# Kernel tuning notes

Measured on AMD Instinct MI355X. Metric: run time of the kernel, lower is better.

Reference implementation:

```python
import jax, jax.numpy as jnp
import numpy as np

B, S, T = 128, 512, 128
E, He, Ed, H = 512, 512, 512, 512


def setup_inputs() -> dict:
    key = jax.random.key(0)
    ks = jax.random.split(key, 13)
    w = lambda k, shape: jax.random.normal(k, shape, jnp.float32) * 0.02
    return {
        "trg_embed": jax.random.normal(ks[0], (B, T, E), jnp.float32),
        "edit_representation_final": jax.random.normal(ks[1], (1, B, 2 * Ed), jnp.float32),
        "edit_representation_cell_state": jax.random.normal(ks[2], (1, B, 2 * Ed), jnp.float32),
        "encoder_hidden": jax.random.normal(ks[3], (B, S, 2 * He), jnp.float32),
        "encoder_final": jax.random.normal(ks[4], (1, B, 2 * He), jnp.float32),
        "encoder_cell_state": jax.random.normal(ks[5], (1, B, 2 * He), jnp.float32),
        "src_mask": jnp.ones((B, 1, S), dtype=bool),
        "W_key": w(ks[6], (2 * He, H)),
        "W_query": w(ks[7], (H, H)),
        "w_energy": w(ks[8], (H,)),
        "W_bridge": w(ks[9], (2 * He + 2 * Ed, H)),
        "b_bridge": jnp.zeros((H,), jnp.float32),
        "W_ih": w(ks[10], (4 * H, E + 2 * He + 2 * Ed)),
        "W_hh": w(ks[11], (4 * H, H)),
        "b_ih": jnp.zeros((4 * H,), jnp.float32),
        "b_hh": jnp.zeros((4 * H,), jnp.float32),
        "W_pre": w(ks[12], (H, H + 2 * He + E)),
    }


def reference(trg_embed, edit_representation_final, edit_representation_cell_state,
              encoder_hidden, encoder_final, encoder_cell_state, src_mask,
              W_key, W_query, w_energy, W_bridge, b_bridge,
              W_ih, W_hh, b_ih, b_hh, W_pre):
    # bridge: init hidden / cell from final encoder + edit states  [1,B,H]
    h0 = jnp.tanh(jnp.concatenate([encoder_final, edit_representation_final], -1) @ W_bridge + b_bridge)
    c0 = jnp.tanh(jnp.concatenate([encoder_cell_state, edit_representation_cell_state], -1) @ W_bridge + b_bridge)
    proj_key = encoder_hidden @ W_key              # [B,S,H] (computed once)
    edit_flat = edit_representation_final[0]       # [B,2*Ed]
    mask = src_mask[:, 0, :]                       # [B,S]
    bias = b_ih + b_hh

    def step(carry, x_t):
        h, c = carry                               # [B,H] each
        # Bahdanau attention
        q = h @ W_query                            # [B,H]
        scores = jnp.tanh(q[:, None, :] + proj_key) @ w_energy   # [B,S]
        scores = jnp.where(mask, scores, -jnp.inf)
        alphas = jax.nn.softmax(scores, axis=-1)
        context = jnp.einsum('bs,bsd->bd', alphas, encoder_hidden)  # [B,2*He]
        # LSTM cell (torch gate order: i, f, g, o)
        rnn_in = jnp.concatenate([x_t, context, edit_flat], -1)
        gates = rnn_in @ W_ih.T + h @ W_hh.T + bias
        i_g, f_g, g_g, o_g = jnp.split(gates, 4, axis=-1)
        c_new = jax.nn.sigmoid(f_g) * c + jax.nn.sigmoid(i_g) * jnp.tanh(g_g)
        h_new = jax.nn.sigmoid(o_g) * jnp.tanh(c_new)
        # pre-output projection (dropout in eval mode = identity)
        pre = jnp.concatenate([x_t, h_new, context], -1) @ W_pre.T
        return (h_new, c_new), (h_new, pre)

    (h_last, c_last), (states, pre_outs) = jax.lax.scan(
        step, (h0[0], c0[0]), jnp.swapaxes(trg_embed, 0, 1))
    decoder_states = jnp.swapaxes(states, 0, 1)       # [B,T,H]
    pre_output_vectors = jnp.swapaxes(pre_outs, 0, 1) # [B,T,H]
    return decoder_states, h_last[None], pre_output_vectors
```

## Files before the change

kernel.cpp:

```cpp
#include <hip/hip_runtime.h>
#include <hip/hip_bf16.h>

typedef unsigned short u16;
typedef unsigned int u32;
typedef unsigned char u8;

typedef __attribute__((ext_vector_type(8))) __bf16 bf16x8;
typedef __attribute__((ext_vector_type(4))) float f32x4;
typedef __attribute__((ext_vector_type(2))) float f32x2;

__device__ __forceinline__ float fast_tanh(float x){
    float e = __expf(2.0f*x);
    return 1.0f - 2.0f/(e+1.0f);
}
__device__ __forceinline__ float fast_sigmoid(float x){
    return 1.0f/(1.0f+__expf(-x));
}
__device__ __forceinline__ float bflo(u32 u){ return __uint_as_float(u<<16); }
__device__ __forceinline__ float bfhi(u32 u){ return __uint_as_float(u & 0xffff0000u); }
__device__ __forceinline__ float bf2f(u16 u){ return __uint_as_float(((u32)u)<<16); }
__device__ __forceinline__ u16 f2bf(float v){
    __hip_bfloat16 h = __float2bfloat16(v);
    return *reinterpret_cast<u16*>(&h);
}
__device__ __forceinline__ f32x2 fp8lo(u32 u){ return __builtin_amdgcn_cvt_pk_f32_fp8(u, false); }
__device__ __forceinline__ f32x2 fp8hi(u32 u){ return __builtin_amdgcn_cvt_pk_f32_fp8(u, true); }

__device__ __forceinline__ void gridbar(int* cnt, int* gate, int e){
    __syncthreads();
    if (threadIdx.x == 0){
        int prev = __hip_atomic_fetch_add(cnt, 1, __ATOMIC_ACQ_REL, __HIP_MEMORY_SCOPE_AGENT);
        if (prev == e*256 - 1)
            __hip_atomic_store(gate, e, __ATOMIC_RELEASE, __HIP_MEMORY_SCOPE_AGENT);
        while (__hip_atomic_load(gate, __ATOMIC_RELAXED, __HIP_MEMORY_SCOPE_AGENT) < e)
            __builtin_amdgcn_s_sleep(8);
        (void)__hip_atomic_load(gate, __ATOMIC_ACQUIRE, __HIP_MEMORY_SCOPE_AGENT);
    }
    __syncthreads();
}

__device__ __forceinline__ void pairbar(int* pflags, int e){
    __syncthreads();
    if (threadIdx.x == 0){
        __hip_atomic_store(&pflags[blockIdx.x*32], e, __ATOMIC_RELEASE, __HIP_MEMORY_SCOPE_AGENT);
        int partner = (blockIdx.x ^ 1)*32;
        while (__hip_atomic_load(&pflags[partner], __ATOMIC_RELAXED, __HIP_MEMORY_SCOPE_AGENT) < e)
            __builtin_amdgcn_s_sleep(2);
        (void)__hip_atomic_load(&pflags[partner], __ATOMIC_ACQUIRE, __HIP_MEMORY_SCOPE_AGENT);
    }
    __syncthreads();
}

template<int C_MODE, int HAS_BIAS>
__global__ __launch_bounds__(256) void mfma_gemm(
    const u16* __restrict__ A, int lda,
    const u16* __restrict__ Bw, int ldb,
    const float* __restrict__ bias,
    void* __restrict__ Cp, long ldc, int K)
{
    __shared__ u16 Ash[128*64];
    __shared__ u16 Bsh[128*64];
    const int tid  = threadIdx.x;
    const int w    = tid >> 6;
    const int lane = tid & 63;
    const int wr   = w >> 1, wc = w & 1;
    const int row0 = blockIdx.y * 128, col0 = blockIdx.x * 128;

    f32x4 acc[4][4];
    #pragma unroll
    for (int i = 0; i < 4; i++)
        #pragma unroll
        for (int j = 0; j < 4; j++)
            acc[i][j] = f32x4{0.f,0.f,0.f,0.f};

    for (int k0 = 0; k0 < K; k0 += 64) {
        #pragma unroll
        for (int it = 0; it < 4; it++) {
            int j = it*256 + tid;
            int row = j >> 3, s = j & 7;
            const u16* src = A + (size_t)(row0 + row) * lda + k0 + ((s ^ (row & 7)) << 3);
            __builtin_amdgcn_global_load_lds(
                (const __attribute__((address_space(1))) unsigned int*)src,
                (__attribute__((address_space(3))) unsigned int*)(Ash + (size_t)(it*256 + w*64)*8),
                16, 0, 0);
        }
        #pragma unroll
        for (int it = 0; it < 4; it++) {
            int j = it*256 + tid;
            int row = j >> 3, s = j & 7;
            const u16* src = Bw + (size_t)(col0 + row) * ldb + k0 + ((s ^ (row & 7)) << 3);
            __builtin_amdgcn_global_load_lds(
                (const __attribute__((address_space(1))) unsigned int*)src,
                (__attribute__((address_space(3))) unsigned int*)(Bsh + (size_t)(it*256 + w*64)*8),
                16, 0, 0);
        }
        __syncthreads();
        #pragma unroll
        for (int kh = 0; kh < 2; kh++) {
            bf16x8 af[4], bg[4];
            #pragma unroll
            for (int f = 0; f < 4; f++) {
                int row = wr*64 + f*16 + (lane & 15);
                int slot = (kh*4 + (lane >> 4)) ^ (row & 7);
                af[f] = *(const bf16x8*)(Ash + row*64 + slot*8);
                int nn = wc*64 + f*16 + (lane & 15);
                int slot2 = (kh*4 + (lane >> 4)) ^ (nn & 7);
                bg[f] = *(const bf16x8*)(Bsh + nn*64 + slot2*8);
            }
            #pragma unroll
            for (int fm = 0; fm < 4; fm++)
                #pragma unroll
                for (int fn = 0; fn < 4; fn++)
                    acc[fm][fn] = __builtin_amdgcn_mfma_f32_16x16x32_bf16(af[fm], bg[fn], acc[fm][fn], 0, 0, 0);
        }
        __syncthreads();
    }

    #pragma unroll
    for (int fm = 0; fm < 4; fm++) {
        #pragma unroll
        for (int fn = 0; fn < 4; fn++) {
            int col = col0 + wc*64 + fn*16 + (lane & 15);
            #pragma unroll
            for (int r = 0; r < 4; r++) {
                int row = row0 + wr*64 + fm*16 + ((lane >> 4)<<2) + r;
                float v = acc[fm][fn][r];
                if (HAS_BIAS) v += bias[col];
                if (C_MODE == 1)
                    ((u16*)Cp)[(size_t)row * ldc + col] = f2bf(v);
                else
                    ((float*)Cp)[(((size_t)(row & 127)) << 16) + ((size_t)(row >> 7) << 9) + col] = v;
            }
        }
    }
}

__global__ __launch_bounds__(512, 1) void k_mega(
    u16* __restrict__ pre_in,
    const u16* __restrict__ Wq_t,
    const u8*  __restrict__ pk8,
    const float* __restrict__ we_g,
    const u8*  __restrict__ enc8,
    const u16* __restrict__ Wg,
    const u16* __restrict__ edit_part,
    u16* __restrict__ gates_part,
    float* __restrict__ scores_g,
    u16* __restrict__ h_glob,
    float* __restrict__ cbuf,
    float* __restrict__ out_states,
    float* __restrict__ out_hlast,
    int* __restrict__ bar)
{
    __shared__ float  hs[512];
    __shared__ float2 qw[512];
    __shared__ float  al[512];
    __shared__ float  red[16];
    __shared__ float  spp[512];
    __shared__ float  cp[16*512];
    __shared__ u16 Ash[8192];
    __shared__ u16 Bsh[8192];
    int* cnt    = bar;
    int* gate   = bar + 32;
    int* pflags = bar + 64;
    const int bid = blockIdx.x, tid = threadIdx.x;
    const int w = tid >> 6, lane = tid & 63;
    const int b = bid >> 1, half = bid & 1;
    const int cb = bid & 15, ks = bid >> 4;
    const int wr = w >> 2, wc = w & 3;

    for (int t = 0; t < 129; t++) {
        if (t == 0) {
            hs[tid] = bf2f(h_glob[b*512 + tid]);
        } else {
            const int j = tid;
            float g4[4];
            #pragma unroll
            for (int g = 0; g < 4; g++) {
                float s = bf2f(edit_part[b*2048 + g*512 + j]);
                #pragma unroll
                for (int kk = 0; kk < 16; kk++)
                    s += bf2f(gates_part[(size_t)kk*262144 + b*2048 + g*512 + j]);
                g4[g] = s;
            }
            float c  = cbuf[(size_t)(t & 1)*65536 + b*512 + j];
            float cn = fast_sigmoid(g4[1])*c + fast_sigmoid(g4[0])*fast_tanh(g4[2]);
            float hn = fast_sigmoid(g4[3])*fast_tanh(cn);
            cbuf[(size_t)((t+1) & 1)*65536 + b*512 + j] = cn;
            hs[j] = hn;
            u16 hb = f2bf(hn);
            h_glob[b*512 + j] = hb;
            pre_in[(size_t)(t-1)*262144 + b*2048 + 1536 + j] = hb;
            out_states[(size_t)b*65536 + (size_t)(t-1)*512 + j] = hn;
            if (t == 128) out_hlast[b*512 + j] = hn;
        }
        if (t == 128) break;
        __syncthreads();
        {
            const int j = tid;
            const uint4* row = (const uint4*)(Wq_t + (size_t)j*512);
            float a = 0.f;
            #pragma unroll 8
            for (int c8 = 0; c8 < 64; c8++) {
                uint4 u = row[c8];
                int k = c8*8;
                a += hs[k+0]*bflo(u.x) + hs[k+1]*bfhi(u.x)
                   + hs[k+2]*bflo(u.y) + hs[k+3]*bfhi(u.y)
                   + hs[k+4]*bflo(u.z) + hs[k+5]*bfhi(u.z)
                   + hs[k+6]*bflo(u.w) + hs[k+7]*bfhi(u.w);
            }
            qw[j] = make_float2(a, we_g[j]);
        }
        __syncthreads();
        {
            const int si = tid & 255, kh2 = tid >> 8;
            const int s = half*256 + si;
            const uint4* prow = (const uint4*)(pk8 + ((size_t)(b*512 + s))*512 + (size_t)kh2*256);
            float acc = 0.f;
            #pragma unroll 4
            for (int c16 = 0; c16 < 16; c16++) {
                uint4 u = prow[c16];
                int kb = kh2*256 + c16*16;
                f32x2 p0, p1;
                p0 = fp8lo(u.x); p1 = fp8hi(u.x);
                acc += fast_tanh(qw[kb+0].x + p0.x)*qw[kb+0].y;
                acc += fast_tanh(qw[kb+1].x + p0.y)*qw[kb+1].y;
                acc += fast_tanh(qw[kb+2].x + p1.x)*qw[kb+2].y;
                acc += fast_tanh(qw[kb+3].x + p1.y)*qw[kb+3].y;
                p0 = fp8lo(u.y); p1 = fp8hi(u.y);
                acc += fast_tanh(qw[kb+4].x + p0.x)*qw[kb+4].y;
                acc += fast_tanh(qw[kb+5].x + p0.y)*qw[kb+5].y;
                acc += fast_tanh(qw[kb+6].x + p1.x)*qw[kb+6].y;
                acc += fast_tanh(qw[kb+7].x + p1.y)*qw[kb+7].y;
                p0 = fp8lo(u.z); p1 = fp8hi(u.z);
                acc += fast_tanh(qw[kb+8].x + p0.x)*qw[kb+8].y;
                acc += fast_tanh(qw[kb+9].x + p0.y)*qw[kb+9].y;
                acc += fast_tanh(qw[kb+10].x + p1.x)*qw[kb+10].y;
                acc += fast_tanh(qw[kb+11].x + p1.y)*qw[kb+11].y;
                p0 = fp8lo(u.w); p1 = fp8hi(u.w);
                acc += fast_tanh(qw[kb+12].x + p0.x)*qw[kb+12].y;
                acc += fast_tanh(qw[kb+13].x + p0.y)*qw[kb+13].y;
                acc += fast_tanh(qw[kb+14].x + p1.x)*qw[kb+14].y;
                acc += fast_tanh(qw[kb+15].x + p1.y)*qw[kb+15].y;
            }
            spp[tid] = acc;
        }
        __syncthreads();
        if (tid < 256)
            scores_g[b*512 + half*256 + tid] = spp[tid] + spp[256 + tid];
        pairbar(pflags, t + 1);

        {
            float sc = scores_g[b*512 + tid];
            float m = sc;
            #pragma unroll
            for (int o = 32; o; o >>= 1) m = fmaxf(m, __shfl_xor(m, o));
            if (lane == 0) red[w] = m;
            __syncthreads();
            m = red[0];
            #pragma unroll
            for (int i = 1; i < 8; i++) m = fmaxf(m, red[i]);
            float p = __expf(sc - m);
            float sm = p;
            #pragma unroll
            for (int o = 32; o; o >>= 1) sm += __shfl_xor(sm, o);
            if (lane == 0) red[8 + w] = sm;
            __syncthreads();
            sm = red[8];
            #pragma unroll
            for (int i = 1; i < 8; i++) sm += red[8 + i];
            al[tid] = p * (1.f / sm);
        }
        __syncthreads();
        {
            const int ch = tid & 31, sg = tid >> 5;
            const uint4* eb = (const uint4*)(enc8 + (size_t)b*524288 + (size_t)half*512 + (size_t)ch*16);
            float c[16];
            #pragma unroll
            for (int e = 0; e < 16; e++) c[e] = 0.f;
            #pragma unroll 4
            for (int s2 = 0; s2 < 32; s2++) {
                int s = sg*32 + s2;
                uint4 u = eb[(size_t)s*64];
                float a = al[s];
                f32x2 p;
                p = fp8lo(u.x); c[0] += a*p.x; c[1] += a*p.y;
                p = fp8hi(u.x); c[2] += a*p.x; c[3] += a*p.y;
                p = fp8lo(u.y); c[4] += a*p.x; c[5] += a*p.y;
                p = fp8hi(u.y); c[6] += a*p.x; c[7] += a*p.y;
                p = fp8lo(u.z); c[8] += a*p.x; c[9] += a*p.y;
                p = fp8hi(u.z); c[10]+= a*p.x; c[11]+= a*p.y;
                p = fp8lo(u.w); c[12]+= a*p.x; c[13]+= a*p.y;
                p = fp8hi(u.w); c[14]+= a*p.x; c[15]+= a*p.y;
            }
            #pragma unroll
            for (int e = 0; e < 16; e++)
                cp[e*512 + sg*32 + ch] = c[e];
        }
        __syncthreads();
        {
            const int ch = tid >> 4, e = tid & 15;
            float v = 0.f;
            #pragma unroll
            for (int g = 0; g < 16; g++) v += cp[e*512 + g*32 + ch];
            pre_in[(size_t)t*262144 + b*2048 + 512 + half*512 + tid] = f2bf(v);
        }
        gridbar(cnt, gate, 2*t + 1);

        {
            const int col0 = cb*128;
            const u16* prow_t = pre_in + (size_t)t*262144;
            f32x4 acc[4][2];
            #pragma unroll
            for (int i = 0; i < 4; i++) { acc[i][0] = f32x4{0.f,0.f,0.f,0.f}; acc[i][1] = f32x4{0.f,0.f,0.f,0.f}; }
            #pragma unroll
            for (int kt = 0; kt < 2; kt++) {
                const int k0 = ks*128 + kt*64;
                #pragma unroll
                for (int it = 0; it < 2; it++) {
                    int jj2 = it*512 + tid;
                    int row = jj2 >> 3, ss = jj2 & 7;
                    int gk = (ss ^ (row & 7)) << 3;
                    const u16* srcA = (ks < 12)
                        ? prow_t + (size_t)row*2048 + k0 + gk
                        : h_glob + (size_t)row*512 + (k0 - 1536) + gk;
                    __builtin_amdgcn_global_load_lds(
                        (const __attribute__((address_space(1))) unsigned int*)srcA,
                        (__attribute__((address_space(3))) unsigned int*)(Ash + (size_t)(it*512 + w*64)*8),
                        16, 0, 0);
                }
                #pragma unroll
                for (int it = 0; it < 2; it++) {
                    int jj2 = it*512 + tid;
                    int row = jj2 >> 3, ss = jj2 & 7;
                    int gk = (ss ^ (row & 7)) << 3;
                    const u16* srcB = Wg + (size_t)(col0 + row)*2048 + k0 + gk;
                    __builtin_amdgcn_global_load_lds(
                        (const __attribute__((address_space(1))) unsigned int*)srcB,
                        (__attribute__((address_space(3))) unsigned int*)(Bsh + (size_t)(it*512 + w*64)*8),
                        16, 0, 0);
                }
                __syncthreads();
                #pragma unroll
                for (int kh = 0; kh < 2; kh++) {
                    bf16x8 af[4], bg[2];
                    #pragma unroll
                    for (int f = 0; f < 4; f++) {
                        int row = wr*64 + f*16 + (lane & 15);
                        int slot = (kh*4 + (lane >> 4)) ^ (row & 7);
                        af[f] = *(const bf16x8*)(Ash + row*64 + slot*8);
                    }
                    #pragma unroll
                    for (int f = 0; f < 2; f++) {
                        int nn = wc*32 + f*16 + (lane & 15);
                        int slot2 = (kh*4 + (lane >> 4)) ^ (nn & 7);
                        bg[f] = *(const bf16x8*)(Bsh + nn*64 + slot2*8);
                    }
                    #pragma unroll
                    for (int fm = 0; fm < 4; fm++)
                        #pragma unroll
                        for (int fn = 0; fn < 2; fn++)
                            acc[fm][fn] = __builtin_amdgcn_mfma_f32_16x16x32_bf16(af[fm], bg[fn], acc[fm][fn], 0, 0, 0);
                }
                __syncthreads();
            }
            u16* gp = gates_part + (size_t)ks*262144;
            #pragma unroll
            for (int fm = 0; fm < 4; fm++)
                #pragma unroll
                for (int fn = 0; fn < 2; fn++) {
                    int cl = col0 + wc*32 + fn*16 + (lane & 15);
                    #pragma unroll
                    for (int r = 0; r < 4; r++) {
                        int bb = wr*64 + fm*16 + ((lane >> 4) << 2) + r;
                        gp[(size_t)bb*2048 + cl] = f2bf(acc[fm][fn][r]);
                    }
                }
        }
        gridbar(cnt, gate, 2*t + 2);
    }
}

__global__ __launch_bounds__(256) void k_cvt_bf16(const float4* __restrict__ in, ushort4* __restrict__ out, int n4){
    int i = blockIdx.x*256 + threadIdx.x;
    if (i >= n4) return;
    float4 v = in[i];
    ushort4 o;
    o.x = f2bf(v.x); o.y = f2bf(v.y); o.z = f2bf(v.z); o.w = f2bf(v.w);
    out[i] = o;
}

__global__ __launch_bounds__(256) void k_cvt_fp8_f32(const float4* __restrict__ in, uint2* __restrict__ out, int n8){
    int i = blockIdx.x*256 + threadIdx.x;
    if (i >= n8) return;
    float4 v0 = in[2*i], v1 = in[2*i+1];
    u32 lo = 0, hi = 0;
    lo = __builtin_amdgcn_cvt_pk_fp8_f32(v0.x, v0.y, lo, false);
    lo = __builtin_amdgcn_cvt_pk_fp8_f32(v0.z, v0.w, lo, true);
    hi = __builtin_amdgcn_cvt_pk_fp8_f32(v1.x, v1.y, hi, false);
    hi = __builtin_amdgcn_cvt_pk_fp8_f32(v1.z, v1.w, hi, true);
    out[i] = make_uint2(lo, hi);
}

__global__ __launch_bounds__(256) void k_cvt_fp8_bf16(const uint4* __restrict__ in, uint2* __restrict__ out, int n8){
    int i = blockIdx.x*256 + threadIdx.x;
    if (i >= n8) return;
    uint4 u = in[i];
    u32 lo = 0, hi = 0;
    lo = __builtin_amdgcn_cvt_pk_fp8_f32(bflo(u.x), bfhi(u.x), lo, false);
    lo = __builtin_amdgcn_cvt_pk_fp8_f32(bflo(u.y), bfhi(u.y), lo, true);
    hi = __builtin_amdgcn_cvt_pk_fp8_f32(bflo(u.z), bfhi(u.z), hi, false);
    hi = __builtin_amdgcn_cvt_pk_fp8_f32(bflo(u.w), bfhi(u.w), hi, true);
    out[i] = make_uint2(lo, hi);
}

__global__ __launch_bounds__(256) void k_bias(const float* __restrict__ a, const float* __restrict__ b, float* __restrict__ o){
    int i = blockIdx.x*256 + threadIdx.x;
    o[i] = a[i] + b[i];
}

__global__ __launch_bounds__(256) void k_cvt_slice(
    u16* __restrict__ out, const float* __restrict__ in,
    int kshift, int ldi, int koff, int ldo, int obase)
{
    int i = blockIdx.x*256 + threadIdx.x;
    int n = i >> kshift, k = i & ((1 << kshift) - 1);
    out[(size_t)n*ldo + obase + k] = f2bf(in[(size_t)n*ldi + koff + k]);
}

__global__ __launch_bounds__(256) void k_tr_bf16(u16* __restrict__ out, const float* __restrict__ in, int K, int N){
    __shared__ float t[32][33];
    int k0 = blockIdx.x*32, n0 = blockIdx.y*32;
    int tx = threadIdx.x & 31, ty = threadIdx.x >> 5;
    for (int i = ty; i < 32; i += 8)
        t[i][tx] = in[(size_t)(k0+i)*N + n0 + tx];
    __syncthreads();
    for (int i = ty; i < 32; i += 8)
        out[(size_t)(n0+i)*K + k0 + tx] = f2bf(t[tx][i]);
}

__global__ __launch_bounds__(256) void k_build_prex(const float4* __restrict__ trg4, u16* __restrict__ pre_in){
    int i = blockIdx.x*256 + threadIdx.x;
    float4 v = trg4[i];
    int kq = i & 127, tt = (i >> 7) & 127, bb = i >> 14;
    ushort4 o;
    o.x = f2bf(v.x); o.y = f2bf(v.y); o.z = f2bf(v.z); o.w = f2bf(v.w);
    *(ushort4*)&pre_in[((size_t)tt*128 + bb)*2048 + kq*4] = o;
}

__global__ __launch_bounds__(256) void k_bridge(
    const float* __restrict__ encf, const float* __restrict__ editf,
    const float* __restrict__ encc, const float* __restrict__ editc,
    const float* __restrict__ Wb, const float* __restrict__ bb,
    u16* __restrict__ h_glob, float* __restrict__ cbuf)
{
    int tid = blockIdx.x*256 + threadIdx.x;
    int sel = tid >> 16;
    int rem = tid & 65535;
    int b = rem >> 9, j = rem & 511;
    const float* s1 = sel ? encc : encf;
    const float* s2 = sel ? editc : editf;
    float acc = bb[j];
    for (int k = 0; k < 1024; k++) acc += s1[b*1024+k] * Wb[k*512 + j];
    for (int k = 0; k < 1024; k++) acc += s2[b*1024+k] * Wb[(1024+k)*512 + j];
    float v = fast_tanh(acc);
    if (sel) cbuf[65536 + rem] = v;
    else     h_glob[rem] = f2bf(v);
}

extern "C" void kernel_launch(void* const* d_in, const int* in_sizes, int n_in,
                              void* d_out, int out_size, void* d_ws, size_t ws_size,
                              hipStream_t stream)
{
    const float* trg      = (const float*)d_in[0];
    const float* editf    = (const float*)d_in[1];
    const float* editc    = (const float*)d_in[2];
    const float* enc      = (const float*)d_in[3];
    const float* encf     = (const float*)d_in[4];
    const float* encc     = (const float*)d_in[5];
    const float* W_key    = (const float*)d_in[7];
    const float* W_query  = (const float*)d_in[8];
    const float* w_energy = (const float*)d_in[9];
    const float* W_bridge = (const float*)d_in[10];
    const float* b_bridge = (const float*)d_in[11];
    const float* W_ih     = (const float*)d_in[12];
    const float* W_hh     = (const float*)d_in[13];
    const float* b_ih     = (const float*)d_in[14];
    const float* b_hh     = (const float*)d_in[15];
    const float* W_pre    = (const float*)d_in[16];
    (void)in_sizes; (void)n_in; (void)out_size; (void)ws_size;

    char* ws = (char*)d_ws;
    size_t off = 0;
    auto alloc = [&](size_t bytes)->char* {
        char* p = ws + off;
        off = (off + bytes + 255) & ~(size_t)255;
        return p;
    };

    u16* enc_b      = (u16*)alloc((size_t)67108864*2);
    u16* pk_b       = (u16*)alloc((size_t)33554432*2);
    u8*  enc8       = (u8*) alloc((size_t)67108864);
    u8*  pk8        = (u8*) alloc((size_t)33554432);
    u16* pre_in     = (u16*)alloc((size_t)33554432*2);
    u16* edit_b     = (u16*)alloc((size_t)131072*2);
    u16* edit_part  = (u16*)alloc((size_t)262144*2);
    u16* Wgfull     = (u16*)alloc((size_t)4194304*2);
    u16* Wedit      = (u16*)alloc((size_t)2097152*2);
    u16* Wp_all     = (u16*)alloc((size_t)1048576*2);
    u16* Wq_t       = (u16*)alloc((size_t)262144*2);
    u16* Wk_t       = (u16*)alloc((size_t)524288*2);
    u16* h_glob     = (u16*)alloc((size_t)65536*2);
    float* cbuf       = (float*)alloc((size_t)131072*4);
    float* bias_comb  = (float*)alloc((size_t)2048*4);
    float* scores_g   = (float*)alloc((size_t)65536*4);
    u16*   gates_part = (u16*)alloc((size_t)4194304*2);
    int*   bar        = (int*)alloc((size_t)(64 + 256*32)*4);

    hipMemsetAsync(bar, 0, (size_t)(64 + 256*32)*4, stream);

    k_cvt_bf16<<<65536, 256, 0, stream>>>((const float4*)enc,   (ushort4*)enc_b,  16777216);
    k_cvt_fp8_f32<<<32768, 256, 0, stream>>>((const float4*)enc, (uint2*)enc8, 8388608);
    k_cvt_bf16<<<128,   256, 0, stream>>>((const float4*)editf, (ushort4*)edit_b, 32768);
    k_bias<<<8, 256, 0, stream>>>(b_ih, b_hh, bias_comb);

    k_cvt_slice<<<4096, 256, 0, stream>>>(Wgfull, W_ih,  9,  2560, 0,    2048, 0);
    k_cvt_slice<<<8192, 256, 0, stream>>>(Wgfull, W_ih,  10, 2560, 512,  2048, 512);
    k_cvt_slice<<<4096, 256, 0, stream>>>(Wgfull, W_hh,  9,  512,  0,    2048, 1536);
    k_cvt_slice<<<8192, 256, 0, stream>>>(Wedit,  W_ih,  10, 2560, 1536, 1024, 0);
    k_cvt_slice<<<1024, 256, 0, stream>>>(Wp_all, W_pre, 9,  2048, 0,    2048, 0);
    k_cvt_slice<<<2048, 256, 0, stream>>>(Wp_all, W_pre, 10, 2048, 1024, 2048, 512);
    k_cvt_slice<<<1024, 256, 0, stream>>>(Wp_all, W_pre, 9,  2048, 512,  2048, 1536);
    k_tr_bf16<<<dim3(16,16), 256, 0, stream>>>(Wq_t, W_query, 512, 512);
    k_tr_bf16<<<dim3(32,16), 256, 0, stream>>>(Wk_t, W_key, 1024, 512);

    k_build_prex<<<8192, 256, 0, stream>>>((const float4*)trg, pre_in);

    mfma_gemm<1,1><<<dim3(16,1), 256, 0, stream>>>(edit_b, 1024, Wedit, 1024,
        bias_comb, edit_part, 2048, 1024);
    mfma_gemm<1,0><<<dim3(4,512), 256, 0, stream>>>(enc_b, 1024, Wk_t, 1024,
        nullptr, pk_b, 512, 1024);
    k_cvt_fp8_bf16<<<16384, 256, 0, stream>>>((const uint4*)pk_b, (uint2*)pk8, 4194304);

    k_bridge<<<512, 256, 0, stream>>>(encf, editf, encc, editc, W_bridge, b_bridge, h_glob, cbuf);

    float* out_states = (float*)d_out;
    float* out_hlast  = (float*)d_out + 8388608;
    float* out_pre    = (float*)d_out + 8454144;

    k_mega<<<256, 512, 0, stream>>>(pre_in, Wq_t, pk8, w_energy, enc8, Wgfull,
        edit_part, gates_part, scores_g, h_glob, cbuf, out_states, out_hlast, bar);

    mfma_gemm<2,0><<<dim3(4,128), 256, 0, stream>>>(pre_in, 2048, Wp_all, 2048,
        nullptr, out_pre, 0, 2048);
}
```

Before: 13.45 ms.

## Double persistent kernel block size and use a hierarchical grid barrier

Moves the persistent decoder kernel from 512 to 1024 threads per block. The query projection, attention scores and context reduction are split across more threads, with extra LDS partial sums. The per-step gate GEMM uses smaller 32x32 warp tiles. Gate partials are stored interleaved so each LSTM thread can read all four gates in one 8-byte load. The grid barrier becomes two-level (eight group counters feeding one global counter) with a shorter sleep, to reduce atomic contention. In exchange there are more __syncthreads per step, more register pressure at 1024 threads, and idle threads in the LSTM phase.

```diff
diff --git a/kernel.cpp b/kernel.cpp
--- a/kernel.cpp
+++ b/kernel.cpp
@@ -26,14 +26,21 @@
 __device__ __forceinline__ f32x2 fp8lo(u32 u){ return __builtin_amdgcn_cvt_pk_f32_fp8(u, false); }
 __device__ __forceinline__ f32x2 fp8hi(u32 u){ return __builtin_amdgcn_cvt_pk_f32_fp8(u, true); }
 
-__device__ __forceinline__ void gridbar(int* cnt, int* gate, int e){
+__device__ __forceinline__ void gridbar(int* bar, int e){
     __syncthreads();
     if (threadIdx.x == 0){
-        int prev = __hip_atomic_fetch_add(cnt, 1, __ATOMIC_ACQ_REL, __HIP_MEMORY_SCOPE_AGENT);
-        if (prev == e*256 - 1)
-            __hip_atomic_store(gate, e, __ATOMIC_RELEASE, __HIP_MEMORY_SCOPE_AGENT);
+        const int g = blockIdx.x & 7;
+        int* gcnt = bar + g*32;
+        int* gall = bar + 256;
+        int* gate = bar + 288;
+        int prev = __hip_atomic_fetch_add(gcnt, 1, __ATOMIC_ACQ_REL, __HIP_MEMORY_SCOPE_AGENT);
+        if (prev == e*32 - 1){
+            int pg = __hip_atomic_fetch_add(gall, 1, __ATOMIC_ACQ_REL, __HIP_MEMORY_SCOPE_AGENT);
+            if (pg == e*8 - 1)
+                __hip_atomic_store(gate, e, __ATOMIC_RELEASE, __HIP_MEMORY_SCOPE_AGENT);
+        }
         while (__hip_atomic_load(gate, __ATOMIC_RELAXED, __HIP_MEMORY_SCOPE_AGENT) < e)
-            __builtin_amdgcn_s_sleep(8);
+            __builtin_amdgcn_s_sleep(4);
         (void)__hip_atomic_load(gate, __ATOMIC_ACQUIRE, __HIP_MEMORY_SCOPE_AGENT);
     }
     __syncthreads();
@@ -135,7 +142,7 @@
     }
 }
 
-__global__ __launch_bounds__(512, 1) void k_mega(
+__global__ __launch_bounds__(1024, 4) void k_mega(
     u16* __restrict__ pre_in,
     const u16* __restrict__ Wq_t,
     const u8*  __restrict__ pk8,
@@ -152,39 +159,40 @@
     int* __restrict__ bar)
 {
     __shared__ float  hs[512];
+    __shared__ float  qp[1024];
     __shared__ float2 qw[512];
     __shared__ float  al[512];
-    __shared__ float  red[16];
-    __shared__ float  spp[512];
-    __shared__ float  cp[16*512];
+    __shared__ float  red[32];
+    __shared__ float  spp[1024];
+    __shared__ float  cp[16*32*17];
     __shared__ u16 Ash[8192];
     __shared__ u16 Bsh[8192];
-    int* cnt    = bar;
-    int* gate   = bar + 32;
-    int* pflags = bar + 64;
+    int* pflags = bar + 320;
     const int bid = blockIdx.x, tid = threadIdx.x;
     const int w = tid >> 6, lane = tid & 63;
     const int b = bid >> 1, half = bid & 1;
     const int cb = bid & 15, ks = bid >> 4;
-    const int wr = w >> 2, wc = w & 3;
+    const int wr = w >> 2, wc2 = w & 3;
 
     for (int t = 0; t < 129; t++) {
         if (t == 0) {
-            hs[tid] = bf2f(h_glob[b*512 + tid]);
-        } else {
+            if (tid < 512) hs[tid] = bf2f(h_glob[b*512 + tid]);
+        } else if (tid < 512) {
             const int j = tid;
-            float g4[4];
-            #pragma unroll
-            for (int g = 0; g < 4; g++) {
-                float s = bf2f(edit_part[b*2048 + g*512 + j]);
-                #pragma unroll
-                for (int kk = 0; kk < 16; kk++)
-                    s += bf2f(gates_part[(size_t)kk*262144 + b*2048 + g*512 + j]);
-                g4[g] = s;
+            float g0 = bf2f(edit_part[b*2048 + j]);
+            float g1 = bf2f(edit_part[b*2048 + 512 + j]);
+            float g2 = bf2f(edit_part[b*2048 + 1024 + j]);
+            float g3 = bf2f(edit_part[b*2048 + 1536 + j]);
+            const uint2* gp2 = (const uint2*)(gates_part + ((size_t)b*512 + j)*4);
+            #pragma unroll
+            for (int kk = 0; kk < 16; kk++) {
+                uint2 u = gp2[(size_t)kk*65536];
+                g0 += bflo(u.x); g1 += bfhi(u.x);
+                g2 += bflo(u.y); g3 += bfhi(u.y);
             }
             float c  = cbuf[(size_t)(t & 1)*65536 + b*512 + j];
-            float cn = fast_sigmoid(g4[1])*c + fast_sigmoid(g4[0])*fast_tanh(g4[2]);
-            float hn = fast_sigmoid(g4[3])*fast_tanh(cn);
+            float cn = fast_sigmoid(g1)*c + fast_sigmoid(g0)*fast_tanh(g2);
+            float hn = fast_sigmoid(g3)*fast_tanh(cn);
             cbuf[(size_t)((t+1) & 1)*65536 + b*512 + j] = cn;
             hs[j] = hn;
             u16 hb = f2bf(hn);
@@ -196,30 +204,32 @@
         if (t == 128) break;
         __syncthreads();
         {
-            const int j = tid;
-            const uint4* row = (const uint4*)(Wq_t + (size_t)j*512);
+            const int j = tid & 511, kh3 = tid >> 9;
+            const uint4* row = (const uint4*)(Wq_t + (size_t)j*512 + (size_t)kh3*256);
             float a = 0.f;
             #pragma unroll 8
-            for (int c8 = 0; c8 < 64; c8++) {
+            for (int c8 = 0; c8 < 32; c8++) {
                 uint4 u = row[c8];
-                int k = c8*8;
+                int k = kh3*256 + c8*8;
                 a += hs[k+0]*bflo(u.x) + hs[k+1]*bfhi(u.x)
                    + hs[k+2]*bflo(u.y) + hs[k+3]*bfhi(u.y)
                    + hs[k+4]*bflo(u.z) + hs[k+5]*bfhi(u.z)
                    + hs[k+6]*bflo(u.w) + hs[k+7]*bfhi(u.w);
             }
-            qw[j] = make_float2(a, we_g[j]);
-        }
+            qp[tid] = a;
+        }
+        __syncthreads();
+        if (tid < 512) qw[tid] = make_float2(qp[tid] + qp[512 + tid], we_g[tid]);
         __syncthreads();
         {
-            const int si = tid & 255, kh2 = tid >> 8;
+            const int si = tid & 255, kq = tid >> 8;
             const int s = half*256 + si;
-            const uint4* prow = (const uint4*)(pk8 + ((size_t)(b*512 + s))*512 + (size_t)kh2*256);
+            const uint4* prow = (const uint4*)(pk8 + ((size_t)(b*512 + s))*512 + (size_t)kq*128);
             float acc = 0.f;
-            #pragma unroll 4
-            for (int c16 = 0; c16 < 16; c16++) {
+            #pragma unroll
+            for (int c16 = 0; c16 < 8; c16++) {
                 uint4 u = prow[c16];
-                int kb = kh2*256 + c16*16;
+                int kb = kq*128 + c16*16;
                 f32x2 p0, p1;
                 p0 = fp8lo(u.x); p1 = fp8hi(u.x);
                 acc += fast_tanh(qw[kb+0].x + p0.x)*qw[kb+0].y;
@@ -246,11 +256,13 @@
         }
         __syncthreads();
         if (tid < 256)
-            scores_g[b*512 + half*256 + tid] = spp[tid] + spp[256 + tid];
+            scores_g[b*512 + half*256 + tid] = spp[tid] + spp[256+tid] + spp[512+tid] + spp[768+tid];
         pairbar(pflags, t + 1);
 
+        float p_keep;
         {
-            float sc = scores_g[b*512 + tid];
+            const int s = tid & 511;
+            float sc = scores_g[b*512 + s];
             float m = sc;
             #pragma unroll
             for (int o = 32; o; o >>= 1) m = fmaxf(m, __shfl_xor(m, o));
@@ -258,17 +270,17 @@
             __syncthreads();
             m = red[0];
             #pragma unroll
-            for (int i = 1; i < 8; i++) m = fmaxf(m, red[i]);
-            float p = __expf(sc - m);
-            float sm = p;
+            for (int i = 1; i < 16; i++) m = fmaxf(m, red[i]);
+            p_keep = __expf(sc - m);
+            float sm = p_keep;
             #pragma unroll
             for (int o = 32; o; o >>= 1) sm += __shfl_xor(sm, o);
-            if (lane == 0) red[8 + w] = sm;
+            if (lane == 0) red[16 + w] = sm;
             __syncthreads();
-            sm = red[8];
-            #pragma unroll
-            for (int i = 1; i < 8; i++) sm += red[8 + i];
-            al[tid] = p * (1.f / sm);
+            sm = red[16];
+            #pragma unroll
+            for (int i = 17; i < 24; i++) sm += red[i];
+            al[s] = p_keep * (1.f / sm);
         }
         __syncthreads();
         {
@@ -278,8 +290,8 @@
             #pragma unroll
             for (int e = 0; e < 16; e++) c[e] = 0.f;
             #pragma unroll 4
-            for (int s2 = 0; s2 < 32; s2++) {
-                int s = sg*32 + s2;
+            for (int s2 = 0; s2 < 16; s2++) {
+                int s = sg*16 + s2;
                 uint4 u = eb[(size_t)s*64];
                 float a = al[s];
                 f32x2 p;
@@ -293,70 +305,63 @@
                 p = fp8hi(u.w); c[14]+= a*p.x; c[15]+= a*p.y;
             }
             #pragma unroll
-            for (int e = 0; e < 16; e++)
-                cp[e*512 + sg*32 + ch] = c[e];
-        }
-        __syncthreads();
-        {
+            for (int e = 0; e < 16; e++) c[e] += __shfl_xor(c[e], 32);
+            if (lane < 32) {
+                #pragma unroll
+                for (int e = 0; e < 16; e++)
+                    cp[(w*32 + ch)*17 + e] = c[e];
+            }
+        }
+        __syncthreads();
+        if (tid < 512) {
             const int ch = tid >> 4, e = tid & 15;
             float v = 0.f;
             #pragma unroll
-            for (int g = 0; g < 16; g++) v += cp[e*512 + g*32 + ch];
+            for (int g = 0; g < 16; g++) v += cp[(g*32 + ch)*17 + e];
             pre_in[(size_t)t*262144 + b*2048 + 512 + half*512 + tid] = f2bf(v);
         }
-        gridbar(cnt, gate, 2*t + 1);
+        gridbar(bar, 2*t + 1);
 
         {
             const int col0 = cb*128;
             const u16* prow_t = pre_in + (size_t)t*262144;
-            f32x4 acc[4][2];
-            #pragma unroll
-            for (int i = 0; i < 4; i++) { acc[i][0] = f32x4{0.f,0.f,0.f,0.f}; acc[i][1] = f32x4{0.f,0.f,0.f,0.f}; }
+            f32x4 acc[2][2];
+            acc[0][0] = f32x4{0.f,0.f,0.f,0.f}; acc[0][1] = f32x4{0.f,0.f,0.f,0.f};
+            acc[1][0] = f32x4{0.f,0.f,0.f,0.f}; acc[1][1] = f32x4{0.f,0.f,0.f,0.f};
             #pragma unroll
             for (int kt = 0; kt < 2; kt++) {
                 const int k0 = ks*128 + kt*64;
-                #pragma unroll
-                for (int it = 0; it < 2; it++) {
-                    int jj2 = it*512 + tid;
-                    int row = jj2 >> 3, ss = jj2 & 7;
-                    int gk = (ss ^ (row & 7)) << 3;
+                {
+                    int row = tid >> 3, sl = tid & 7;
+                    int gk = (sl ^ (row & 7)) << 3;
                     const u16* srcA = (ks < 12)
                         ? prow_t + (size_t)row*2048 + k0 + gk
                         : h_glob + (size_t)row*512 + (k0 - 1536) + gk;
                     __builtin_amdgcn_global_load_lds(
                         (const __attribute__((address_space(1))) unsigned int*)srcA,
-                        (__attribute__((address_space(3))) unsigned int*)(Ash + (size_t)(it*512 + w*64)*8),
+                        (__attribute__((address_space(3))) unsigned int*)(Ash + (size_t)w*512),
                         16, 0, 0);
-                }
-                #pragma unroll
-                for (int it = 0; it < 2; it++) {
-                    int jj2 = it*512 + tid;
-                    int row = jj2 >> 3, ss = jj2 & 7;
-                    int gk = (ss ^ (row & 7)) << 3;
                     const u16* srcB = Wg + (size_t)(col0 + row)*2048 + k0 + gk;
                     __builtin_amdgcn_global_load_lds(
                         (const __attribute__((address_space(1))) unsigned int*)srcB,
-                        (__attribute__((address_space(3))) unsigned int*)(Bsh + (size_t)(it*512 + w*64)*8),
+                        (__attribute__((address_space(3))) unsigned int*)(Bsh + (size_t)w*512),
                         16, 0, 0);
                 }
                 __syncthreads();
                 #pragma unroll
                 for (int kh = 0; kh < 2; kh++) {
-                    bf16x8 af[4], bg[2];
+                    bf16x8 af[2], bg[2];
                     #pragma unroll
-                    for (int f = 0; f < 4; f++) {
-                        int row = wr*64 + f*16 + (lane & 15);
+                    for (int f = 0; f < 2; f++) {
+                        int row = wr*32 + f*16 + (lane & 15);
                         int slot = (kh*4 + (lane >> 4)) ^ (row & 7);
                         af[f] = *(const bf16x8*)(Ash + row*64 + slot*8);
-                    }
-                    #pragma unroll
-                    for (int f = 0; f < 2; f++) {
-                        int nn = wc*32 + f*16 + (lane & 15);
+                        int nn = wc2*32 + f*16 + (lane & 15);
                         int slot2 = (kh*4 + (lane >> 4)) ^ (nn & 7);
                         bg[f] = *(const bf16x8*)(Bsh + nn*64 + slot2*8);
                     }
                     #pragma unroll
-                    for (int fm = 0; fm < 4; fm++)
+                    for (int fm = 0; fm < 2; fm++)
                         #pragma unroll
                         for (int fn = 0; fn < 2; fn++)
                             acc[fm][fn] = __builtin_amdgcn_mfma_f32_16x16x32_bf16(af[fm], bg[fn], acc[fm][fn], 0, 0, 0);
@@ -365,18 +370,19 @@
             }
             u16* gp = gates_part + (size_t)ks*262144;
             #pragma unroll
-            for (int fm = 0; fm < 4; fm++)
+            for (int fm = 0; fm < 2; fm++)
                 #pragma unroll
                 for (int fn = 0; fn < 2; fn++) {
-                    int cl = col0 + wc*32 + fn*16 + (lane & 15);
+                    int c = col0 + wc2*32 + fn*16 + (lane & 15);
+                    int cidx = (c & 511)*4 + (c >> 9);
                     #pragma unroll
                     for (int r = 0; r < 4; r++) {
-                        int bb = wr*64 + fm*16 + ((lane >> 4) << 2) + r;
-                        gp[(size_t)bb*2048 + cl] = f2bf(acc[fm][fn][r]);
+                        int bb = wr*32 + fm*16 + ((lane >> 4) << 2) + r;
+                        gp[(size_t)bb*2048 + cidx] = f2bf(acc[fm][fn][r]);
                     }
                 }
         }
-        gridbar(cnt, gate, 2*t + 2);
+        gridbar(bar, 2*t + 2);
     }
 }
 
@@ -514,9 +520,9 @@
     float* bias_comb  = (float*)alloc((size_t)2048*4);
     float* scores_g   = (float*)alloc((size_t)65536*4);
     u16*   gates_part = (u16*)alloc((size_t)4194304*2);
-    int*   bar        = (int*)alloc((size_t)(64 + 256*32)*4);
-
-    hipMemsetAsync(bar, 0, (size_t)(64 + 256*32)*4, stream);
+    int*   bar        = (int*)alloc((size_t)(320 + 256*32)*4);
+
+    hipMemsetAsync(bar, 0, (size_t)(320 + 256*32)*4, stream);
 
     k_cvt_bf16<<<65536, 256, 0, stream>>>((const float4*)enc,   (ushort4*)enc_b,  16777216);
     k_cvt_fp8_f32<<<32768, 256, 0, stream>>>((const float4*)enc, (uint2*)enc8, 8388608);
@@ -547,7 +553,7 @@
     float* out_hlast  = (float*)d_out + 8388608;
     float* out_pre    = (float*)d_out + 8454144;
 
-    k_mega<<<256, 512, 0, stream>>>(pre_in, Wq_t, pk8, w_energy, enc8, Wgfull,
+    k_mega<<<256, 1024, 0, stream>>>(pre_in, Wq_t, pk8, w_energy, enc8, Wgfull,
         edit_part, gates_part, scores_g, h_glob, cbuf, out_states, out_hlast, bar);
 
     mfma_gemm<2,0><<<dim3(4,128), 256, 0, stream>>>(pre_in, 2048, Wp_all, 2048,
```

Result: slower. 14.31 ms (+6.5%).
